# Kernel tuning notes

Hardware: AMD Instinct MI355X
Metric: run time of the kernel (lower is better)

## Reference

```python
import jax, jax.numpy as jnp
import numpy as np

TEMP = 0.05
BG_KNN = 50
POSK = 3
BAL_W = 0.15
P = 32768   # num proxies in memory bank
D = 256     # feature dim
C = 8       # num cameras (proxy p has camera p % C, pseudo-label p // C)
N = 65536   # dataset size
B = 256     # batch


def setup_inputs() -> dict:
    key = jax.random.key(0)
    k1, k2, k3, k4 = jax.random.split(key, 4)
    mem = jax.random.normal(k1, (P, D), jnp.float32)
    mem = mem / jnp.linalg.norm(mem, axis=1, keepdims=True)  # L2-normalized bank
    features = jax.random.normal(k2, (B, D), jnp.float32)
    all_proxy_label = jax.random.randint(k3, (N,), 0, P, jnp.int32)
    all_pseudo_label = all_proxy_label // C          # consistent with label_proxies layout
    targets = jax.random.randint(k4, (B,), 0, N, jnp.int32)
    cams = all_proxy_label[targets] % C              # each sample's camera owns its target proxy
    Pc = P // C
    cam_proxies = (jnp.arange(C)[:, None] + C * jnp.arange(Pc)[None, :]).astype(jnp.int32)   # [C, Pc]
    label_proxies = (jnp.arange(P // C)[:, None] * C + jnp.arange(C)[None, :]).astype(jnp.int32)  # [num_ids, C]
    return dict(features=features, targets=targets, cams=cams, epoch=0,
                global_memory=mem, all_pseudo_label=all_pseudo_label,
                all_proxy_label=all_proxy_label, cam_proxies=cam_proxies,
                label_proxies=label_proxies)


def _cam_mean_sum(per_sample, cams, num_cams):
    # original: for each camera, mean loss over that camera's samples, then sum over cameras
    s = jax.ops.segment_sum(per_sample, cams, num_segments=num_cams)
    n = jax.ops.segment_sum(jnp.ones_like(per_sample), cams, num_segments=num_cams)
    return jnp.where(n > 0, s / jnp.maximum(n, 1.0), 0.0).sum()


def _forward(features, global_memory, targets, cams, all_pseudo_label,
             all_proxy_label, cam_proxies, label_proxies):
    pseudo_y = all_pseudo_label[targets]      # [B]
    prx = all_proxy_label[targets]            # [B]
    num_cams = cam_proxies.shape[0]
    Bsz = features.shape[0]
    rows = jnp.arange(Bsz)

    # ExemplarMemory: score = features @ memory^T; backward treats memory as constant
    score = features @ jax.lax.stop_gradient(global_memory).T   # [B, P]
    inputs = score / TEMP

    # --- intra-camera loss: log-softmax over this sample's camera proxies ---
    cam_prx = cam_proxies[cams]                                   # [B, Pc]
    sel = jnp.take_along_axis(inputs, cam_prx, axis=1)            # [B, Pc]
    mask = (cam_prx == prx[:, None]).astype(inputs.dtype)
    intra = -(jax.nn.log_softmax(sel, axis=1) * mask).sum(axis=1)

    # --- cross-camera proxy-associate loss: positives + bg_knn hardest negatives ---
    pos = label_proxies[pseudo_y]                                 # [B, K]
    K = pos.shape[1]
    temp = jax.lax.stop_gradient(inputs).at[rows[:, None], pos].set(10000.0)
    _, top_idx = jax.lax.top_k(temp, BG_KNN + K)                  # descending: positives first
    sel2 = jnp.take_along_axis(inputs, top_idx, axis=1)           # [B, bg_knn+K]
    tgt2 = jnp.concatenate([jnp.full((K,), 1.0 / K, inputs.dtype),
                            jnp.zeros((BG_KNN,), inputs.dtype)])
    cross = -(jax.nn.log_softmax(sel2, axis=1) * tgt2).sum(axis=1)

    # --- online camera-wise NN-enhance loss ---
    mem = jax.lax.stop_gradient(global_memory)
    sims = BAL_W * jax.lax.stop_gradient(score) + (1.0 - BAL_W) * (mem[prx] @ mem.T)  # [B, P]
    sims_by_cam = sims[:, cam_proxies]                            # [B, C, Pc]
    arg = jnp.argmax(sims_by_cam, axis=2)                         # [B, C] best proxy per camera
    tops = cam_proxies[jnp.arange(num_cams)[None, :], arg]        # [B, C]
    top_vals = jnp.take_along_axis(sims, tops, axis=1)            # [B, C]
    _, sel_c = jax.lax.top_k(top_vals, POSK)                      # posK strongest camera-tops
    chosen = jnp.take_along_axis(tops, sel_c, axis=1)             # [B, posK]
    sims = sims.at[rows[:, None], chosen].set(10000.0)
    _, top3 = jax.lax.top_k(sims, BG_KNN + POSK)                  # positives first (descending)
    sel3 = jnp.take_along_axis(inputs, top3, axis=1)
    tgt3 = jnp.concatenate([jnp.full((POSK,), 1.0 / POSK, inputs.dtype),
                            jnp.zeros((BG_KNN,), inputs.dtype)])
    online = -(jax.nn.log_softmax(sel3, axis=1) * tgt3).sum(axis=1)

    return (_cam_mean_sum(intra, cams, num_cams)
            + _cam_mean_sum(cross, cams, num_cams)
            + _cam_mean_sum(online, cams, num_cams))


def reference(features, targets, cams, epoch, global_memory, all_pseudo_label,
              all_proxy_label, cam_proxies, label_proxies):
    return _forward(features, global_memory, targets, cams,
                    all_pseudo_label, all_proxy_label, cam_proxies, label_proxies)
```

## Files before the change

### kernel.cpp

```cpp
#include <hip/hip_runtime.h>

#define P_CNT 32768
#define D_DIM 256
#define B_SZ  256
#define NTHR  1024
#define NW    16
#define INVT  20.0f
#define NEG_BIG -3.0e38f

typedef _Float16 half8  __attribute__((ext_vector_type(8)));
typedef _Float16 half4v __attribute__((ext_vector_type(4)));
typedef float    floatx4 __attribute__((ext_vector_type(4)));

__device__ __forceinline__ float blockMax(float v, int tid, float* redW) {
#pragma unroll
  for (int off = 1; off < 64; off <<= 1) v = fmaxf(v, __shfl_xor(v, off));
  if ((tid & 63) == 0) redW[tid >> 6] = v;
  __syncthreads();
  float r = redW[0];
#pragma unroll
  for (int w = 1; w < NW; ++w) r = fmaxf(r, redW[w]);
  __syncthreads();
  return r;
}

__device__ __forceinline__ float blockSum(float v, int tid, float* redW) {
#pragma unroll
  for (int off = 1; off < 64; off <<= 1) v += __shfl_xor(v, off);
  if ((tid & 63) == 0) redW[tid >> 6] = v;
  __syncthreads();
  float r = 0.f;
#pragma unroll
  for (int w = 0; w < NW; ++w) r += redW[w];
  __syncthreads();
  return r;
}

__device__ __forceinline__ unsigned fkey(float v) {
  unsigned bu = __float_as_uint(v);
  return bu ^ ((unsigned)(((int)bu) >> 31) | 0x80000000u);
}

template <typename GetV>
__device__ __forceinline__ void histFindBin(GetV getv, int k, int tid,
                                            int* hist , int* wt ,
                                            int* ibc ,
                                            unsigned& prefixOut, int& prevShiftOut,
                                            int& kremOut) {
  const int lane = tid & 63, wid = tid >> 6;
  int shift = 19, prevShift = 32;
  unsigned prefix = 0;
  int krem = k;
  for (;;) {
    int4* h4 = (int4*)hist;
    h4[tid] = make_int4(0, 0, 0, 0);
    h4[tid + 1024] = make_int4(0, 0, 0, 0);
    __syncthreads();
#pragma unroll
    for (int j = 0; j < 32; ++j) {
      unsigned key = fkey(getv(j));
      bool ok = (prevShift >= 32) || ((key >> prevShift) == prefix);
      if (ok) atomicAdd(&hist[(key >> shift) & 8191], 1);
    }
    __syncthreads();
    int bcnt[8];
    int L = 0;
#pragma unroll
    for (int j = 0; j < 8; ++j) { bcnt[j] = hist[8 * tid + j]; L += bcnt[j]; }
    int S = L;
#pragma unroll
    for (int off = 1; off < 64; off <<= 1) {
      int y = __shfl_down(S, off);
      S += (lane + off < 64) ? y : 0;
    }
    if (lane == 0) wt[wid] = S;
    __syncthreads();
    int aboveW = 0;
    for (int w = wid + 1; w < NW; ++w) aboveW += wt[w];
    const int R = S + aboveW;
    const int aboveR = R - L;
    if (aboveR < krem && krem <= R) {
      int above = aboveR;
      int bsel = -1, csel = 0;
#pragma unroll
      for (int j = 7; j >= 0; --j) {
        if (bsel < 0) {
          if (above + bcnt[j] >= krem) { bsel = 8 * tid + j; csel = bcnt[j]; }
          else above += bcnt[j];
        }
      }
      ibc[0] = bsel; ibc[1] = krem - above; ibc[2] = csel;
    }
    __syncthreads();
    const int bstar = ibc[0];
    krem = ibc[1];
    const int cntT = ibc[2];
    const int gap = prevShift - shift;
    prefix = (prefix << gap) | ((unsigned)bstar & ((1u << gap) - 1u));
    prevShift = shift;
    if (cntT <= 64 || shift == 0) break;
    shift = (shift >= 13) ? (shift - 13) : 0;
    __syncthreads();
  }
  prefixOut = prefix; prevShiftOut = prevShift; kremOut = krem;
}

__global__ void prep_kernel(const float* __restrict__ features,
                            const int* __restrict__ targets,
                            const int* __restrict__ all_prx,
                            const float* __restrict__ mem,
                            float* __restrict__ A2,
                            int* __restrict__ prxArr) {
  const int b = blockIdx.x;
  const int k = threadIdx.x;
  const int t = targets[b];
  const int pr = all_prx[t];
  if (k == 0) prxArr[b] = pr;
  A2[b * D_DIM + k] = features[b * D_DIM + k];
  A2[(B_SZ + b) * D_DIM + k] = mem[(size_t)pr * D_DIM + k];
}

__global__ __launch_bounds__(256) void gemm_mfma(const float* __restrict__ A,
                                                 const float* __restrict__ Bm,
                                                 float* __restrict__ Co) {
  __shared__ _Float16 Ah[128][32], Al[128][32], Bh[128][32], Bl[128][32];
  const int tid = threadIdx.x;
  const int lane = tid & 63;
  const int wid = tid >> 6;
  const int wr = wid >> 1, wc = wid & 1;
  const int orig = (blockIdx.x & 7) * 128 + (blockIdx.x >> 3);
  const int rowBase = (orig & 3) << 7;
  const int colBase = (orig >> 2) << 7;

  const int trow = tid >> 3;
  const int tseg = tid & 7;

  floatx4 acc[4][4];
#pragma unroll
  for (int i = 0; i < 4; ++i)
#pragma unroll
    for (int j = 0; j < 4; ++j) {
      acc[i][j][0] = 0.f; acc[i][j][1] = 0.f; acc[i][j][2] = 0.f; acc[i][j][3] = 0.f;
    }

  const int fr = lane & 15;
  const int kg = (lane >> 4) << 3;

  for (int step = 0; step < 8; ++step) {
    const int k0 = step << 5;
    float4 sa[4], sb[4];
#pragma unroll
    for (int p = 0; p < 4; ++p) {
      const int r = trow + (p << 5);
      sa[p] = *(const float4*)(A  + (size_t)(rowBase + r) * D_DIM + k0 + tseg * 4);
      sb[p] = *(const float4*)(Bm + (size_t)(colBase + r) * D_DIM + k0 + tseg * 4);
    }
    __syncthreads();
#pragma unroll
    for (int p = 0; p < 4; ++p) {
      const int r = trow + (p << 5);
      float4 v = sa[p];
      half4v h, l;
      h[0] = (_Float16)v.x; l[0] = (_Float16)(v.x - (float)h[0]);
      h[1] = (_Float16)v.y; l[1] = (_Float16)(v.y - (float)h[1]);
      h[2] = (_Float16)v.z; l[2] = (_Float16)(v.z - (float)h[2]);
      h[3] = (_Float16)v.w; l[3] = (_Float16)(v.w - (float)h[3]);
      *(half4v*)&Ah[r][tseg * 4] = h;
      *(half4v*)&Al[r][tseg * 4] = l;
      v = sb[p];
      h[0] = (_Float16)v.x; l[0] = (_Float16)(v.x - (float)h[0]);
      h[1] = (_Float16)v.y; l[1] = (_Float16)(v.y - (float)h[1]);
      h[2] = (_Float16)v.z; l[2] = (_Float16)(v.z - (float)h[2]);
      h[3] = (_Float16)v.w; l[3] = (_Float16)(v.w - (float)h[3]);
      *(half4v*)&Bh[r][tseg * 4] = h;
      *(half4v*)&Bl[r][tseg * 4] = l;
    }
    __syncthreads();
    half8 ah[4], al[4], bh[4], bl[4];
#pragma unroll
    for (int f = 0; f < 4; ++f) {
      ah[f] = *(const half8*)&Ah[wr * 64 + f * 16 + fr][kg];
      al[f] = *(const half8*)&Al[wr * 64 + f * 16 + fr][kg];
      bh[f] = *(const half8*)&Bh[wc * 64 + f * 16 + fr][kg];
      bl[f] = *(const half8*)&Bl[wc * 64 + f * 16 + fr][kg];
    }
#pragma unroll
    for (int fm = 0; fm < 4; ++fm)
#pragma unroll
      for (int fn = 0; fn < 4; ++fn) {
        acc[fm][fn] = __builtin_amdgcn_mfma_f32_16x16x32_f16(ah[fm], bh[fn], acc[fm][fn], 0, 0, 0);
        acc[fm][fn] = __builtin_amdgcn_mfma_f32_16x16x32_f16(ah[fm], bl[fn], acc[fm][fn], 0, 0, 0);
        acc[fm][fn] = __builtin_amdgcn_mfma_f32_16x16x32_f16(al[fm], bh[fn], acc[fm][fn], 0, 0, 0);
      }
  }
  const int rsub = (lane >> 4) << 2;
#pragma unroll
  for (int fm = 0; fm < 4; ++fm)
#pragma unroll
    for (int fn = 0; fn < 4; ++fn) {
      const int r0 = rowBase + wr * 64 + fm * 16 + rsub;
      const int c0 = colBase + wc * 64 + fn * 16 + fr;
#pragma unroll
      for (int r = 0; r < 4; ++r)
        Co[(size_t)(r0 + r) * P_CNT + c0] = acc[fm][fn][r];
    }
}

__global__ __launch_bounds__(NTHR) void persample(const float* __restrict__ OUT,
                                                  const int* __restrict__ cams,
                                                  const int* __restrict__ prxArr,
                                                  float* __restrict__ intraArr,
                                                  float* __restrict__ crossArr,
                                                  float* __restrict__ onlArr) {
  __shared__ int   hist[8192];
  __shared__ int   wt[NW];
  __shared__ int   ibc[4];
  __shared__ float bufV[64];
  __shared__ int   bufI[64];
  __shared__ int   cntS[4];
  __shared__ float redW[NW];
  __shared__ float sv[64];
  __shared__ int   si[64];
  __shared__ float cvW[NW * 8];
  __shared__ int   ciW[NW * 8];
  __shared__ float mw[NW], sw[NW];

  const int b = blockIdx.x;
  const int tid = threadIdx.x;
  const int lane = tid & 63, wid = tid >> 6;
  const float* Srow = OUT + (size_t)b * P_CNT;
  const float* Mrow = OUT + (size_t)(B_SZ + b) * P_CNT;
  const int pr = prxArr[b];
  const int cam = cams[b];
  const int base4 = tid << 2;

  float s[32];
#pragma unroll
  for (int q = 0; q < 8; ++q) {
    float4 f = ((const float4*)Srow)[tid + (q << 10)];
    s[4 * q + 0] = f.x; s[4 * q + 1] = f.y; s[4 * q + 2] = f.z; s[4 * q + 3] = f.w;
  }
  float pmax = NEG_BIG;
#pragma unroll
  for (int j = 0; j < 32; ++j) pmax = fmaxf(pmax, s[j]);
  const float M = blockMax(pmax, tid, redW);

  {
    const bool mine = ((tid & 1) == (cam >> 2));
    const int cc = cam & 3;
    float im = NEG_BIG, is = 0.f;
    if (mine) {
#pragma unroll
      for (int q = 0; q < 8; ++q) {
        float v = (cc == 0) ? s[4 * q] : (cc == 1) ? s[4 * q + 1]
                : (cc == 2) ? s[4 * q + 2] : s[4 * q + 3];
        if (v <= im) is += expf((v - im) * INVT);
        else { is = is * expf((im - v) * INVT) + 1.f; im = v; }
      }
    }
#pragma unroll
    for (int off = 1; off < 64; off <<= 1) {
      float m2 = __shfl_xor(im, off);
      float s2 = __shfl_xor(is, off);
      float Mx = fmaxf(im, m2);
      is = is * expf((im - Mx) * INVT) + s2 * expf((m2 - Mx) * INVT);
      im = Mx;
    }
    if (lane == 0) { mw[wid] = im; sw[wid] = is; }
  }
  const int posBase = pr & ~7;
  if (tid < 8) sv[tid] = Srow[posBase + tid];
  __syncthreads();
  if (tid == 0) {
    float m0 = mw[0], s0 = sw[0];
    for (int w = 1; w < NW; ++w) {
      float Mx = fmaxf(m0, mw[w]);
      s0 = s0 * expf((m0 - Mx) * INVT) + sw[w] * expf((mw[w] - Mx) * INVT);
      m0 = Mx;
    }
    intraArr[b] = -((Srow[pr] - m0) * INVT - logf(s0));
  }

  auto crossVal = [&](int j) -> float {
    int p = base4 + ((j >> 2) << 12) + (j & 3);
    return ((unsigned)(p - posBase) < 8u) ? NEG_BIG : s[j];
  };
  {
    unsigned prefix; int prevShift, krem;
    histFindBin(crossVal, 50, tid, hist, wt, ibc, prefix, prevShift, krem);
    if (tid == 0) cntS[0] = 0;
    __syncthreads();
    float seAbove = 0.f;
#pragma unroll
    for (int j = 0; j < 32; ++j) {
      float v = crossVal(j);
      unsigned keyTop = fkey(v) >> prevShift;
      if (keyTop > prefix) seAbove += expf((v - M) * INVT);
      else if (keyTop == prefix) {
        int p = atomicAdd(&cntS[0], 1);
        if (p < 64) bufV[p] = v;
      }
    }
    seAbove = blockSum(seAbove, tid, redW);
    if (tid < 64) {
      const int n = min(cntS[0], 64);
      const bool valid = (tid < n);
      float vl = valid ? bufV[tid] : NEG_BIG;
      int r = 0, eq = 0;
      for (int m2 = 0; m2 < 64; ++m2) {
        float vm = (m2 < n) ? bufV[m2] : NEG_BIG;
        r += (vm > vl); eq += (vm == vl);
      }
      unsigned long long mb = __ballot(valid && r < krem && krem <= r + eq);
      int selLane = (mb == 0) ? 0 : (int)__ffsll(mb) - 1;
      float vk = __shfl(vl, selLane);
      int rAbove = __shfl(r, selLane);
      float e = (valid && vl > vk) ? expf((vl - M) * INVT) : 0.f;
#pragma unroll
      for (int off = 1; off < 64; off <<= 1) e += __shfl_xor(e, off);
      if (tid == 0) {
        float stot = seAbove + e + (float)(krem - rAbove) * expf((vk - M) * INVT);
        float acc = 0.f;
        for (int p = 0; p < 8; ++p) stot += expf((sv[p] - M) * INVT);
        float lse = logf(stot);
        for (int p = 0; p < 8; ++p) acc += (sv[p] - M) * INVT - lse;
        crossArr[b] = -acc * 0.125f;
      }
    }
  }

#pragma unroll
  for (int q = 0; q < 8; ++q) {
    float4 m2 = ((const float4*)Mrow)[tid + (q << 10)];
    s[4 * q + 0] = 0.15f * s[4 * q + 0] + 0.85f * m2.x;
    s[4 * q + 1] = 0.15f * s[4 * q + 1] + 0.85f * m2.y;
    s[4 * q + 2] = 0.15f * s[4 * q + 2] + 0.85f * m2.z;
    s[4 * q + 3] = 0.15f * s[4 * q + 3] + 0.85f * m2.w;
  }

  {
    float cm[4] = {NEG_BIG, NEG_BIG, NEG_BIG, NEG_BIG};
    int cix[4] = {0x7fffffff, 0x7fffffff, 0x7fffffff, 0x7fffffff};
#pragma unroll
    for (int q = 0; q < 8; ++q) {
#pragma unroll
      for (int c = 0; c < 4; ++c) {
        float v = s[4 * q + c];
        int p = base4 + (q << 12) + c;
        if (v > cm[c]) { cm[c] = v; cix[c] = p; }
      }
    }
    const bool odd = (tid & 1);
    float v8[8]; int i8[8];
#pragma unroll
    for (int c = 0; c < 4; ++c) {
      float ov = __shfl_xor(cm[c], 1); int oi = __shfl_xor(cix[c], 1);
      v8[c]     = odd ? ov : cm[c];   i8[c]     = odd ? oi : cix[c];
      v8[c + 4] = odd ? cm[c] : ov;   i8[c + 4] = odd ? cix[c] : oi;
    }
#pragma unroll
    for (int off = 2; off <= 32; off <<= 1) {
#pragma unroll
      for (int c = 0; c < 8; ++c) {
        float vv = __shfl_xor(v8[c], off);
        int   ii = __shfl_xor(i8[c], off);
        if (vv > v8[c] || (vv == v8[c] && ii < i8[c])) { v8[c] = vv; i8[c] = ii; }
      }
    }
    if (lane < 8) {
#pragma unroll
      for (int c = 0; c < 8; ++c)
        if (lane == c) { cvW[wid * 8 + c] = v8[c]; ciW[wid * 8 + c] = i8[c]; }
    }
    __syncthreads();
    if (tid < 8) {
      float v = cvW[tid]; int ix = ciW[tid];
      for (int w = 1; w < NW; ++w) {
        float v2 = cvW[w * 8 + tid]; int i2 = ciW[w * 8 + tid];
        if (v2 > v || (v2 == v && i2 < ix)) { v = v2; ix = i2; }
      }
      cvW[tid] = v; ciW[tid] = ix;
    }
    __syncthreads();
    if (tid == 0) {
      unsigned used = 0;
      for (int k = 0; k < 3; ++k) {
        float best = NEG_BIG; int bc = 0;
        for (int c = 0; c < 8; ++c)
          if (!((used >> c) & 1u) && cvW[c] > best) { best = cvW[c]; bc = c; }
        used |= 1u << bc;
        si[k] = ciW[bc];
      }
    }
    __syncthreads();
  }
  const int c0 = si[0], c1 = si[1], c2 = si[2];
  __syncthreads();

  auto simsVal = [&](int j) -> float {
    int p = base4 + ((j >> 2) << 12) + (j & 3);
    return (p == c0 || p == c1 || p == c2) ? NEG_BIG : s[j];
  };
  {
    unsigned prefix; int prevShift, krem;
    histFindBin(simsVal, 50, tid, hist, wt, ibc, prefix, prevShift, krem);
    if (tid == 0) { cntS[0] = 0; cntS[1] = 3; }
    __syncthreads();
#pragma unroll
    for (int j = 0; j < 32; ++j) {
      float v = simsVal(j);
      int p = base4 + ((j >> 2) << 12) + (j & 3);
      unsigned keyTop = fkey(v) >> prevShift;
      if (keyTop > prefix) {
        int t = atomicAdd(&cntS[1], 1);
        si[t] = p;
      } else if (keyTop == prefix) {
        int t = atomicAdd(&cntS[0], 1);
        if (t < 64) { bufV[t] = v; bufI[t] = p; }
      }
    }
    __syncthreads();
    if (tid < 64) {
      const int n = min(cntS[0], 64);
      const bool valid = (tid < n);
      float vl = valid ? bufV[tid] : NEG_BIG;
      int il = valid ? bufI[tid] : 0x7fffffff;
      int r = 0, eq = 0, ti = 0;
      for (int m2 = 0; m2 < 64; ++m2) {
        float vm = (m2 < n) ? bufV[m2] : NEG_BIG;
        int im = (m2 < n) ? bufI[m2] : 0x7fffffff;
        r += (vm > vl); eq += (vm == vl);
        ti += (vm == vl && im < il);
      }
      unsigned long long mb = __ballot(valid && r < krem && krem <= r + eq);
      int selLane = (mb == 0) ? 0 : (int)__ffsll(mb) - 1;
      float vk = __shfl(vl, selLane);
      int rAbove = __shfl(r, selLane);
      int tcnt = krem - rAbove;
      bool take = valid && ((vl > vk) || (vl == vk && ti < tcnt));
      if (take) {
        int t = atomicAdd(&cntS[1], 1);
        si[t] = il;
      }
      float v = NEG_BIG;
      if (tid < 53) v = Srow[si[tid]];
      float mm = v;
#pragma unroll
      for (int off = 1; off < 64; off <<= 1) mm = fmaxf(mm, __shfl_xor(mm, off));
      float e = (tid < 53) ? expf((v - mm) * INVT) : 0.f;
      float ss = e;
#pragma unroll
      for (int off = 1; off < 64; off <<= 1) ss += __shfl_xor(ss, off);
      float lse = logf(ss);
      float c = (tid < 3) ? ((v - mm) * INVT - lse) : 0.f;
#pragma unroll
      for (int off = 1; off < 64; off <<= 1) c += __shfl_xor(c, off);
      if (tid == 0) onlArr[b] = -c * (1.0f / 3.0f);
    }
  }
}

__global__ void finalize(const int* __restrict__ cams,
                         const float* __restrict__ ia,
                         const float* __restrict__ ca,
                         const float* __restrict__ oa,
                         float* __restrict__ out) {
  if (blockIdx.x == 0 && threadIdx.x == 0) {
    float s[8] = {}; float n[8] = {};
    for (int b = 0; b < B_SZ; ++b) {
      int c = cams[b];
      s[c] += ia[b] + ca[b] + oa[b];
      n[c] += 1.f;
    }
    float tot = 0.f;
    for (int c = 0; c < 8; ++c)
      if (n[c] > 0.f) tot += s[c] / n[c];
    out[0] = tot;
  }
}

extern "C" void kernel_launch(void* const* d_in, const int* in_sizes, int n_in,
                              void* d_out, int out_size, void* d_ws, size_t ws_size,
                              hipStream_t stream) {
  const float* features = (const float*)d_in[0];
  const int*   targets  = (const int*)d_in[1];
  const int*   cams     = (const int*)d_in[2];
  const float* mem      = (const float*)d_in[4];
  const int*   all_prx  = (const int*)d_in[6];

  float* ws = (float*)d_ws;
  float* A2  = ws;
  float* OUT = ws + 512 * D_DIM;
  float* tail = OUT + (size_t)512 * P_CNT;
  int*   prxArr  = (int*)tail;
  float* intraArr = (float*)(prxArr + B_SZ);
  float* crossArr = intraArr + B_SZ;
  float* onlArr   = crossArr + B_SZ;

  prep_kernel<<<B_SZ, D_DIM, 0, stream>>>(features, targets, all_prx, mem, A2, prxArr);
  gemm_mfma<<<1024, 256, 0, stream>>>(A2, mem, OUT);
  persample<<<B_SZ, NTHR, 0, stream>>>(OUT, cams, prxArr, intraArr, crossArr, onlArr);
  finalize<<<1, 64, 0, stream>>>(cams, intraArr, crossArr, onlArr, (float*)d_out);
}
```

Measured before the change: 162.6 us.

## Replace radix-key histogram top-k search with equal-width value-range histograms

The radix-bit histogram selection over float keys is replaced with equal-width histograms over a value range anchored at the row maximum. The window widens when the k-th element is not found and refines into the selected bin otherwise. Because 13-bit radix bins pack most cosine scores into a few bins, the old search needed several passes; spreading bins over the actual value range should shrink the candidate set in fewer passes. The cost is an extra block max reduction for the second selection, float binning arithmetic, and a possible precision or tie edge case in the bin classification.

```diff
diff --git a/kernel.cpp b/kernel.cpp
--- a/kernel.cpp
+++ b/kernel.cpp
@@ -36,37 +36,62 @@
   return r;
 }
 
-__device__ __forceinline__ unsigned fkey(float v) {
-  unsigned bu = __float_as_uint(v);
-  return bu ^ ((unsigned)(((int)bu) >> 31) | 0x80000000u);
+__device__ __forceinline__ int binOf(float v, float lo, float sc) {
+  float t = (v - lo) * sc;
+  t = fminf(fmaxf(t, 0.0f), 8191.0f);
+  return (int)t;
+}
+
+__device__ __forceinline__ int classify(float v, int depth,
+                                        float lo0, float sc0, int b0,
+                                        float lo1, float sc1, int b1,
+                                        float lo2, float sc2, int b2) {
+  bool eq = true, ab = false;
+  { int bb = binOf(v, lo0, sc0); ab |= eq && (bb > b0); eq = eq && (bb == b0); }
+  if (depth > 1) { int bb = binOf(v, lo1, sc1); ab |= eq && (bb > b1); eq = eq && (bb == b1); }
+  if (depth > 2) { int bb = binOf(v, lo2, sc2); ab |= eq && (bb > b2); eq = eq && (bb == b2); }
+  return ab ? 1 : (eq ? 2 : 0);
 }
 
 template <typename GetV>
-__device__ __forceinline__ void histFindBin(GetV getv, int k, int tid,
-                                            int* hist , int* wt ,
-                                            int* ibc ,
-                                            unsigned& prefixOut, int& prevShiftOut,
-                                            int& kremOut) {
+__device__ __forceinline__ void findBinEW(GetV getv, int k, int tid,
+                                          float hi, float range,
+                                          int* hist, int* wt, int* ibc,
+                                          float& lo0, float& sc0, int& b0,
+                                          float& lo1, float& sc1, int& b1,
+                                          float& lo2, float& sc2, int& b2,
+                                          int& depth, int& kremOut) {
   const int lane = tid & 63, wid = tid >> 6;
-  int shift = 19, prevShift = 32;
-  unsigned prefix = 0;
+  float lo = hi - range, sc = 8192.0f / range;
   int krem = k;
-  for (;;) {
+  depth = 0;
+  for (int guard = 0; guard < 8; ++guard) {
     int4* h4 = (int4*)hist;
     h4[tid] = make_int4(0, 0, 0, 0);
     h4[tid + 1024] = make_int4(0, 0, 0, 0);
+    if (tid == 0) ibc[0] = -2;
     __syncthreads();
 #pragma unroll
     for (int j = 0; j < 32; ++j) {
-      unsigned key = fkey(getv(j));
-      bool ok = (prevShift >= 32) || ((key >> prevShift) == prefix);
-      if (ok) atomicAdd(&hist[(key >> shift) & 8191], 1);
+      float v = getv(j);
+      bool memb = true;
+      if (depth > 0) memb = memb && (binOf(v, lo0, sc0) == b0);
+      if (depth > 1) memb = memb && (binOf(v, lo1, sc1) == b1);
+      if (depth > 2) memb = memb && (binOf(v, lo2, sc2) == b2);
+      if (memb) {
+        int bin = binOf(v, lo, sc);
+        if (bin >= 1) atomicAdd(&hist[bin], 1);
+      }
     }
     __syncthreads();
     int bcnt[8];
     int L = 0;
 #pragma unroll
-    for (int j = 0; j < 8; ++j) { bcnt[j] = hist[8 * tid + j]; L += bcnt[j]; }
+    for (int j = 0; j < 8; ++j) {
+      int bi = 8 * tid + j;
+      int c = (bi >= 1) ? hist[bi] : 0;
+      bcnt[j] = c; L += c;
+    }
     int S = L;
 #pragma unroll
     for (int off = 1; off < 64; off <<= 1) {
@@ -77,8 +102,7 @@
     __syncthreads();
     int aboveW = 0;
     for (int w = wid + 1; w < NW; ++w) aboveW += wt[w];
-    const int R = S + aboveW;
-    const int aboveR = R - L;
+    const int R = S + aboveW, aboveR = R - L;
     if (aboveR < krem && krem <= R) {
       int above = aboveR;
       int bsel = -1, csel = 0;
@@ -93,16 +117,25 @@
     }
     __syncthreads();
     const int bstar = ibc[0];
-    krem = ibc[1];
-    const int cntT = ibc[2];
-    const int gap = prevShift - shift;
-    prefix = (prefix << gap) | ((unsigned)bstar & ((1u << gap) - 1u));
-    prevShift = shift;
-    if (cntT <= 64 || shift == 0) break;
-    shift = (shift >= 13) ? (shift - 13) : 0;
-    __syncthreads();
-  }
-  prefixOut = prefix; prevShiftOut = prevShift; kremOut = krem;
+    const int kin = ibc[1], cntT = ibc[2];
+    __syncthreads();
+    if (bstar < 0) {
+      float hi2 = lo;
+      range = range * 4.0f;
+      lo = hi2 - range; sc = 8192.0f / range;
+      continue;
+    }
+    krem = kin;
+    if (depth == 0)      { lo0 = lo; sc0 = sc; b0 = bstar; }
+    else if (depth == 1) { lo1 = lo; sc1 = sc; b1 = bstar; }
+    else                 { lo2 = lo; sc2 = sc; b2 = bstar; }
+    depth++;
+    if (cntT <= 64 || depth >= 3) break;
+    float w = range / 8192.0f;
+    lo = lo + (float)bstar * w;
+    range = w; sc = 8192.0f / w;
+  }
+  kremOut = krem;
 }
 
 __global__ void prep_kernel(const float* __restrict__ features,
@@ -286,17 +319,19 @@
     return ((unsigned)(p - posBase) < 8u) ? NEG_BIG : s[j];
   };
   {
-    unsigned prefix; int prevShift, krem;
-    histFindBin(crossVal, 50, tid, hist, wt, ibc, prefix, prevShift, krem);
+    float lo0 = 0, sc0 = 0, lo1 = 0, sc1 = 0, lo2 = 0, sc2 = 0;
+    int b0 = 0, b1 = 0, b2 = 0, depth = 0, krem = 0;
+    findBinEW(crossVal, 50, tid, M, 2.0f, hist, wt, ibc,
+              lo0, sc0, b0, lo1, sc1, b1, lo2, sc2, b2, depth, krem);
     if (tid == 0) cntS[0] = 0;
     __syncthreads();
     float seAbove = 0.f;
 #pragma unroll
     for (int j = 0; j < 32; ++j) {
       float v = crossVal(j);
-      unsigned keyTop = fkey(v) >> prevShift;
-      if (keyTop > prefix) seAbove += expf((v - M) * INVT);
-      else if (keyTop == prefix) {
+      int cls = classify(v, depth, lo0, sc0, b0, lo1, sc1, b1, lo2, sc2, b2);
+      if (cls == 1) seAbove += expf((v - M) * INVT);
+      else if (cls == 2) {
         int p = atomicAdd(&cntS[0], 1);
         if (p < 64) bufV[p] = v;
       }
@@ -402,19 +437,26 @@
     return (p == c0 || p == c1 || p == c2) ? NEG_BIG : s[j];
   };
   {
-    unsigned prefix; int prevShift, krem;
-    histFindBin(simsVal, 50, tid, hist, wt, ibc, prefix, prevShift, krem);
+    float pm2 = NEG_BIG;
+#pragma unroll
+    for (int j = 0; j < 32; ++j) pm2 = fmaxf(pm2, simsVal(j));
+    const float Ms = blockMax(pm2, tid, redW);
+
+    float lo0 = 0, sc0 = 0, lo1 = 0, sc1 = 0, lo2 = 0, sc2 = 0;
+    int b0 = 0, b1 = 0, b2 = 0, depth = 0, krem = 0;
+    findBinEW(simsVal, 50, tid, Ms, 0.5f, hist, wt, ibc,
+              lo0, sc0, b0, lo1, sc1, b1, lo2, sc2, b2, depth, krem);
     if (tid == 0) { cntS[0] = 0; cntS[1] = 3; }
     __syncthreads();
 #pragma unroll
     for (int j = 0; j < 32; ++j) {
       float v = simsVal(j);
       int p = base4 + ((j >> 2) << 12) + (j & 3);
-      unsigned keyTop = fkey(v) >> prevShift;
-      if (keyTop > prefix) {
+      int cls = classify(v, depth, lo0, sc0, b0, lo1, sc1, b1, lo2, sc2, b2);
+      if (cls == 1) {
         int t = atomicAdd(&cntS[1], 1);
         si[t] = p;
-      } else if (keyTop == prefix) {
+      } else if (cls == 2) {
         int t = atomicAdd(&cntS[0], 1);
         if (t < 64) { bufV[t] = v; bufI[t] = p; }
       }
```

After: 243.1 us. +49.5%, slower.
